# Optimization experiments

Hardware: AMD Instinct MI355X
Metric: run time of the kernel (lower is better)

The kernel has to match this reference:

```python
import jax, jax.numpy as jnp
import numpy as np

VAR0, VAR1 = 0.1, 0.2
CONF_THR = 0.02
NMS_THR = 0.4
PRE_K = 5000
POST_K = 750
N = 85680


def setup_inputs() -> dict:
    key = jax.random.key(0)
    k0, k1, k2, k3 = jax.random.split(key, 4)
    return {
        "loc": jax.random.normal(k0, (N, 4), jnp.float32),
        "conf": jax.random.uniform(k1, (N, 2), jnp.float32),
        "landmarks": jax.random.normal(k2, (N, 10), jnp.float32),
        "priors": jax.random.uniform(k3, (N, 4), jnp.float32),
        "img_w": 1920,
        "img_h": 1088,
    }


def _decode_boxes(loc, priors):
    # center-size decode -> xyxy
    cxy = priors[:, :2] + loc[:, :2] * VAR0 * priors[:, 2:]
    wh = priors[:, 2:] * jnp.exp(loc[:, 2:] * VAR1)
    return jnp.concatenate([cxy - wh * 0.5, cxy + wh * 0.5], axis=-1)


def _decode_landmarks(lmk, priors):
    pts = lmk.reshape(-1, 5, 2)                       # [N,5,2]
    out = priors[:, None, :2] + pts * VAR0 * priors[:, None, 2:]
    return out.reshape(-1, 10)


def _pairwise_iou(boxes):
    # boxes: [K,4] xyxy
    area = (boxes[:, 2] - boxes[:, 0]) * (boxes[:, 3] - boxes[:, 1])
    lt = jnp.maximum(boxes[:, None, :2], boxes[None, :, :2])  # [K,K,2]
    rb = jnp.minimum(boxes[:, None, 2:], boxes[None, :, 2:])
    wh = jnp.clip(rb - lt, 0.0)
    inter = wh[..., 0] * wh[..., 1]
    union = area[:, None] + area[None, :] - inter
    return inter / jnp.maximum(union, 1e-12)


def _greedy_nms(boxes, valid, thr):
    # boxes already sorted by descending score; valid marks real candidates.
    K = boxes.shape[0]
    iou = _pairwise_iou(boxes)                         # [K,K]
    idx = jnp.arange(K)

    def body(i, keep):
        suppress = keep[i] & (iou[i] > thr) & (idx > i)
        return keep & ~suppress

    return jax.lax.fori_loop(0, K, body, valid)


def reference(loc, conf, landmarks, priors, img_w, img_h):
    w = jnp.float32(img_w)
    h = jnp.float32(img_h)
    bbox_scale = jnp.array([w, h, w, h], jnp.float32)
    lmk_scale = jnp.tile(jnp.array([w, h], jnp.float32), 5)

    boxes = _decode_boxes(loc, priors) * bbox_scale          # [N,4]
    lmk = _decode_landmarks(landmarks, priors) * lmk_scale   # [N,10]
    scores = conf[:, 1]                                      # [N]

    # confidence filter fused into top-k via -inf masking (static shapes)
    masked = jnp.where(scores > CONF_THR, scores, -jnp.inf)
    top_scores, order = jax.lax.top_k(masked, PRE_K)         # [PRE_K]
    boxes_k = boxes[order]
    lmk_k = lmk[order]
    valid_k = top_scores > CONF_THR

    keep = _greedy_nms(boxes_k, valid_k, NMS_THR)            # [PRE_K] bool

    # compact kept rows (already score-sorted) into fixed [POST_K,15]
    rank = jnp.cumsum(keep) - 1
    rows = jnp.concatenate([boxes_k, top_scores[:, None], lmk_k], axis=1)
    dest = jnp.where(keep & (rank < POST_K), rank, POST_K)   # OOB -> dropped
    out = jnp.zeros((POST_K, 15), jnp.float32).at[dest].set(rows, mode="drop")
    return out
```

## Files before the change

kernel.cpp:

```cpp
#include <hip/hip_runtime.h>
#include <hip/hip_bf16.h>
#include <math.h>

#define N_IN 85680
#define PRE_K 5000
#define POST_K 750
#define NW 79
#define NPAD 5056
#define HSIZE 8192
#define CAND_MAX 8192
#define CONF_THR 0.02f
#define NMS_THR 0.4f
#define BITS_THR 0x3CA3D70Bu
#define NGRP 20
#define ZBYTES 66624

typedef unsigned int u32;
typedef unsigned long long u64;

__device__ __forceinline__ int cbase(int k) { return k * (5088 - 32 * k); }

__device__ __forceinline__ float opaquef(float x) { asm volatile("" : "+v"(x)); return x; }

__device__ __forceinline__ u32 bucket_of(u32 bits) {
    u32 b = (bits - BITS_THR) >> 13;
    return b >= HSIZE ? (HSIZE - 1) : b;
}

__global__ __launch_bounds__(256) void zero_kernel(u32* __restrict__ p) {
    int i = blockIdx.x * 256 + threadIdx.x;
    if (i < ZBYTES / 4) p[i] = 0u;
}

__global__ __launch_bounds__(256) void hist_kernel(const float2* __restrict__ conf2,
                                                   u32* __restrict__ hist) {
    __shared__ u32 h[HSIZE];
    for (int b = threadIdx.x; b < HSIZE; b += 256) h[b] = 0u;
    __syncthreads();
    int i = blockIdx.x * 256 + threadIdx.x;
    if (i < N_IN) {
        float s = conf2[i].y;
        if (s > CONF_THR) atomicAdd(&h[bucket_of(__float_as_uint(s))], 1u);
    }
    __syncthreads();
    for (int b = threadIdx.x; b < HSIZE; b += 256) {
        u32 v = h[b];
        if (v) atomicAdd(&hist[b], v);
    }
}

__global__ __launch_bounds__(1024) void scan_kernel(const u32* __restrict__ hist,
                                                    u32* __restrict__ bsel,
                                                    u32* __restrict__ bstart) {
    __shared__ u32 tot[1024];
    int c = threadIdx.x;
    u32 lh[8];
    u32 t = 0;
#pragma unroll
    for (int k = 0; k < 8; ++k) { lh[k] = hist[c * 8 + k]; t += lh[k]; }
    tot[c] = t;
    __syncthreads();
    for (int d = 1; d < 1024; d <<= 1) {
        u32 v = tot[c] + ((c + d < 1024) ? tot[c + d] : 0u);
        __syncthreads();
        tot[c] = v;
        __syncthreads();
    }
    u32 above = (c + 1 < 1024) ? tot[c + 1] : 0u;
    u32 s = above;
    for (int k = 7; k >= 0; --k) { bstart[c * 8 + k] = s; s += lh[k]; }
    if (above < PRE_K && above + t >= PRE_K) {
        u32 cum = above;
        for (int k = 7; k >= 0; --k) {
            cum += lh[k];
            if (cum >= PRE_K) { bsel[0] = (u32)(c * 8 + k); break; }
        }
    }
    if (c == 0 && tot[0] < PRE_K) bsel[0] = 0u;
}

__global__ __launch_bounds__(256) void compact_kernel(const float2* __restrict__ conf2,
                                                      const u32* __restrict__ bsel,
                                                      const u32* __restrict__ bstart,
                                                      u32* __restrict__ bfill,
                                                      u64* __restrict__ cand) {
    int i = blockIdx.x * 256 + threadIdx.x;
    if (i >= N_IN) return;
    float sc = conf2[i].y;
    if (!(sc > CONF_THR)) return;
    u32 bits = __float_as_uint(sc);
    u32 b = bucket_of(bits);
    if (b < bsel[0]) return;
    u32 pos = bstart[b] + atomicAdd(&bfill[b], 1u);
    if (pos < CAND_MAX) cand[pos] = ((u64)bits << 32) | (u64)(u32)(~(u32)i);
}

__global__ __launch_bounds__(256) void rankdec_kernel(const u64* __restrict__ cand,
                                                      const u32* __restrict__ bstart,
                                                      const u32* __restrict__ bfill,
                                                      const u32* __restrict__ bsel,
                                                      const float4* __restrict__ loc4,
                                                      const float4* __restrict__ pri4,
                                                      const float* __restrict__ lmk,
                                                      const int* __restrict__ imw,
                                                      const int* __restrict__ imh,
                                                      float4* __restrict__ rows4,
                                                      float4* __restrict__ boxes,
                                                      u64* __restrict__ validm) {
    u32 bs = bsel[0];
    u32 total = bstart[bs] + bfill[bs];
    if (total > CAND_MAX) total = CAND_MAX;
    float W = (float)(*imw), H = (float)(*imh);
    for (u32 s = blockIdx.x * blockDim.x + threadIdx.x; s < total;
         s += gridDim.x * blockDim.x) {
        u64 key = cand[s];
        u32 b = bucket_of((u32)(key >> 32));
        u32 st = bstart[b];
        u32 en = st + bfill[b];
        if (en > CAND_MAX) en = CAND_MAX;
        u32 r = st;
        for (u32 j = st; j < en; ++j) r += (cand[j] > key) ? 1u : 0u;
        if (r >= PRE_K) continue;
        u32 i = ~(u32)key;
        float score = __uint_as_float((u32)(key >> 32));
        float4 L = loc4[i];
        float4 P = pri4[i];
        float cx = P.x + opaquef((L.x * 0.1f) * P.z);
        float cy = P.y + opaquef((L.y * 0.1f) * P.w);
        float bw = P.z * (float)exp((double)(L.z * 0.2f));
        float bh = P.w * (float)exp((double)(L.w * 0.2f));
        float hw = opaquef(bw * 0.5f), hh = opaquef(bh * 0.5f);
        float x0 = (cx - hw) * W, y0 = (cy - hh) * H;
        float x1 = (cx + hw) * W, y1 = (cy + hh) * H;
        boxes[r] = make_float4(x0, y0, x1, y1);
        float lm[10];
#pragma unroll
        for (int p = 0; p < 5; ++p) {
            float2 q = ((const float2*)lmk)[(size_t)i * 5 + p];
            lm[2 * p]     = (P.x + opaquef((q.x * 0.1f) * P.z)) * W;
            lm[2 * p + 1] = (P.y + opaquef((q.y * 0.1f) * P.w)) * H;
        }
        float4* row = rows4 + (size_t)r * 4;
        row[0] = make_float4(x0, y0, x1, y1);
        row[1] = make_float4(score, lm[0], lm[1], lm[2]);
        row[2] = make_float4(lm[3], lm[4], lm[5], lm[6]);
        row[3] = make_float4(lm[7], lm[8], lm[9], 0.f);
        atomicOr(&validm[r >> 6], 1ull << (r & 63));
    }
}

__global__ __launch_bounds__(256) void mask_kernel(const float4* __restrict__ boxes,
                                                   u64* __restrict__ cmask) {
    __shared__ float4 cb4[4][64];
    int wv = threadIdx.x >> 6, t = threadIdx.x & 63;
    int t64 = blockIdx.x * 4 + wv;
    if (t64 >= NW * (NW + 1) / 2) return;
    int rc = (int)((sqrtf(8.0f * (float)t64 + 1.0f) - 1.0f) * 0.5f);
    while ((rc + 1) * (rc + 2) / 2 <= t64) ++rc;
    while (rc * (rc + 1) / 2 > t64) --rc;
    int cc = t64 - rc * (rc + 1) / 2;
    cb4[wv][t] = boxes[cc * 64 + t];
    int i = rc * 64 + t;
    float4 bi = boxes[i];
    float areai = (bi.z - bi.x) * (bi.w - bi.y);
    u64 word = 0ull;
#pragma unroll 4
    for (int k = 0; k < 64; ++k) {
        float4 bj = cb4[wv][k];
        float areaj = (bj.z - bj.x) * (bj.w - bj.y);
        float ltx = fmaxf(bi.x, bj.x), lty = fmaxf(bi.y, bj.y);
        float rbx = fminf(bi.z, bj.z), rby = fminf(bi.w, bj.w);
        float wx = fmaxf(rbx - ltx, 0.f), wy = fmaxf(rby - lty, 0.f);
        float inter = opaquef(wx * wy);
        float uni = fmaxf(areai + areaj - inter, 1e-12f);
        float iou = inter / uni;
        if (iou > NMS_THR) word |= (1ull << k);
    }
    if (i < PRE_K) cmask[(size_t)(cbase(cc) + (i - 64 * cc))] = word;
}

#define FC(k, q) cmask[(size_t)(cbase(k) + (q) - 64 * (k))]

#define WAITG(need)                                                                   \
    for (;;) {                                                                        \
        u32 d_ = __hip_atomic_load(&doneCnt, __ATOMIC_RELAXED,                        \
                                   __HIP_MEMORY_SCOPE_WORKGROUP);                     \
        if (d_ > (u32)NGRP) { dead = true; break; }                                   \
        if (d_ >= (u32)(need)) break;                                                 \
    }                                                                                 \
    asm volatile("" ::: "memory");

__device__ __forceinline__ u64 nms_solve(u64 valw, u64 sup, u64 dlow) {
    u64 keep = valw & ~__ballot(sup != 0ull);
    for (;;) {
        u64 conm = __ballot((dlow & keep) != 0ull);
        u64 cm = conm & keep;
        if (cm == 0ull) break;
        u64 U = keep & ~conm;
        u64 rem = __ballot((dlow & U) != 0ull) & keep;
        keep &= ~rem;
    }
    return keep;
}

__global__ __launch_bounds__(512) void reduce_scatter_kernel(const u64* __restrict__ cmask,
                                                             const u64* __restrict__ validm,
                                                             const float* __restrict__ rows,
                                                             float* __restrict__ out) {
    int tid = threadIdx.x;
    int g = tid >> 6, lane = tid & 63;
    __shared__ u64 keepAll[96];
    __shared__ u32 totG[32];
    __shared__ u32 doneCnt;
    __shared__ u32 wpref[96];
    for (int k = tid; k < 96; k += 512) keepAll[k] = 0ull;
    if (tid == 0) doneCnt = 0u;
    __syncthreads();
    u64 lmask = (1ull << lane) - 1ull;

    for (int s = 0; s < 3; ++s) {
        int G = s * 8 + g;
        if (G >= NGRP) break;
        int w0 = 4 * G;
        int nwg = NW - w0; if (nwg > 4) nwg = 4;
        int q0 = 64 * w0 + lane;
        int q1 = q0 + 64;
        int q2 = q0 + 128;
        int q3 = (nwg > 3) ? (q0 + 192) : q0;
        u64 t00 = FC(w0, q0);
        u64 t10 = (nwg > 1) ? FC(w0, q1) : 0ull;
        u64 t11 = (nwg > 1) ? FC(w0 + 1, q1) : 0ull;
        u64 t20 = (nwg > 2) ? FC(w0, q2) : 0ull;
        u64 t21 = (nwg > 2) ? FC(w0 + 1, q2) : 0ull;
        u64 t22 = (nwg > 2) ? FC(w0 + 2, q2) : 0ull;
        u64 t30 = (nwg > 3) ? FC(w0, q3) : 0ull;
        u64 t31 = (nwg > 3) ? FC(w0 + 1, q3) : 0ull;
        u64 t32 = (nwg > 3) ? FC(w0 + 2, q3) : 0ull;
        u64 t33 = (nwg > 3) ? FC(w0 + 3, q3) : 0ull;
        u64 v0 = validm[w0];
        u64 v1 = (nwg > 1) ? validm[w0 + 1] : 0ull;
        u64 v2 = (nwg > 2) ? validm[w0 + 2] : 0ull;
        u64 v3 = (nwg > 3) ? validm[w0 + 3] : 0ull;
        u64 sup0 = 0, sup1 = 0, sup2 = 0, sup3 = 0;
        bool dead = false;

        int d0 = 0;
        u64 c00=0,c01=0,c02=0,c03=0,c10=0,c11=0,c12=0,c13=0;
        if (w0 > 0) {
            c00 = FC(0, q0); c01 = FC(0, q1); c02 = FC(0, q2); c03 = FC(0, q3);
            c10 = FC(1, q0); c11 = FC(1, q1); c12 = FC(1, q2); c13 = FC(1, q3);
        }
        asm volatile("" ::: "memory");
        while (d0 < w0) {
            int d1 = d0 + 2;
            u64 n00=0,n01=0,n02=0,n03=0,n10=0,n11=0,n12=0,n13=0;
            if (d1 < w0) {
                n00 = FC(d1, q0);     n01 = FC(d1, q1);     n02 = FC(d1, q2);     n03 = FC(d1, q3);
                n10 = FC(d1 + 1, q0); n11 = FC(d1 + 1, q1); n12 = FC(d1 + 1, q2); n13 = FC(d1 + 1, q3);
            }
            asm volatile("" ::: "memory");
            WAITG(((d0 + 1) >> 2) + 1)
            if (dead) break;
            u64 ka = keepAll[d0], kb = keepAll[d0 + 1];
            sup0 |= (ka & c00) | (kb & c10);
            sup1 |= (ka & c01) | (kb & c11);
            sup2 |= (ka & c02) | (kb & c12);
            sup3 |= (ka & c03) | (kb & c13);
            c00=n00;c01=n01;c02=n02;c03=n03;c10=n10;c11=n11;c12=n12;c13=n13;
            d0 = d1;
        }
        if (!dead) {
            __builtin_amdgcn_s_setprio(1);
            u32 tp = (G > 0) ? totG[G - 1] : 0u;
            u64 k0 = 0, k1 = 0, k2 = 0, k3 = 0;
            if (tp < POST_K) {
                k0 = nms_solve(v0, sup0, t00 & lmask);
                sup1 |= k0 & t10; sup2 |= k0 & t20; sup3 |= k0 & t30;
                k1 = nms_solve(v1, sup1, t11 & lmask);
                sup2 |= k1 & t21; sup3 |= k1 & t31;
                k2 = nms_solve(v2, sup2, t22 & lmask);
                sup3 |= k2 & t32;
                k3 = nms_solve(v3, sup3, t33 & lmask);
            }
            if (lane == 0) {
                keepAll[w0]     = k0;
                keepAll[w0 + 1] = k1;
                keepAll[w0 + 2] = k2;
                keepAll[w0 + 3] = k3;
                u32 tk = tp + (u32)(__popcll(k0) + __popcll(k1) + __popcll(k2) + __popcll(k3));
                totG[G] = tk;
                asm volatile("s_waitcnt lgkmcnt(0)" ::: "memory");
                __hip_atomic_store(&doneCnt,
                                   (tk >= POST_K) ? (u32)(NGRP + 9) : (u32)(G + 1),
                                   __ATOMIC_RELAXED, __HIP_MEMORY_SCOPE_WORKGROUP);
            }
            __builtin_amdgcn_s_setprio(0);
        } else {
            break;
        }
    }
    __syncthreads();

    if (tid == 0) {
        u32 s = 0;
        for (int w = 0; w < NW; ++w) { wpref[w] = s; s += (u32)__popcll(keepAll[w]); }
        wpref[NW] = s;
    }
    __syncthreads();
    u32 totk = wpref[NW]; if (totk > POST_K) totk = POST_K;
    for (int r = tid; r < PRE_K; r += 512) {
        int w = r >> 6, b = r & 63;
        u64 kw = keepAll[w];
        if ((kw >> b) & 1ull) {
            u32 rank = wpref[w] + (u32)__popcll(kw & ((1ull << b) - 1ull));
            if (rank < POST_K) {
                const float* src = rows + (size_t)r * 16;
                float* dst = out + (size_t)rank * 15;
#pragma unroll
                for (int c2 = 0; c2 < 15; ++c2) dst[c2] = src[c2];
            }
        }
    }
    for (int r = (int)totk + tid; r < POST_K; r += 512) {
        float* dst = out + (size_t)r * 15;
#pragma unroll
        for (int c2 = 0; c2 < 15; ++c2) dst[c2] = 0.f;
    }
}

extern "C" void kernel_launch(void* const* d_in, const int* in_sizes, int n_in,
                              void* d_out, int out_size, void* d_ws, size_t ws_size,
                              hipStream_t stream) {
    const float* loc = (const float*)d_in[0];
    const float2* conf2 = (const float2*)d_in[1];
    const float* lmk = (const float*)d_in[2];
    const float* pri = (const float*)d_in[3];
    const int* imw = (const int*)d_in[4];
    const int* imh = (const int*)d_in[5];
    float* out = (float*)d_out;
    char* base = (char*)d_ws;

    u32* hist   = (u32*)(base + 0);
    u32* bfill  = (u32*)(base + 32768);
    u32* bsel   = (u32*)(base + 65536);
    u64* validm = (u64*)(base + 65600);
    u32* bstart = (u32*)(base + 67648);
    u64* cand   = (u64*)(base + 100416);
    float* rows = (float*)(base + 165952);
    float4* boxes = (float4*)(base + 485952);
    u64* cmask  = (u64*)(base + 566848);

    zero_kernel<<<(ZBYTES / 4 + 255) / 256, 256, 0, stream>>>((u32*)base);

    hist_kernel<<<(N_IN + 255) / 256, 256, 0, stream>>>(conf2, hist);
    scan_kernel<<<1, 1024, 0, stream>>>(hist, bsel, bstart);
    compact_kernel<<<(N_IN + 255) / 256, 256, 0, stream>>>(conf2, bsel, bstart, bfill, cand);
    rankdec_kernel<<<48, 256, 0, stream>>>(cand, bstart, bfill, bsel, (const float4*)loc,
                                           (const float4*)pri, lmk, imw, imh,
                                           (float4*)rows, boxes, validm);
    mask_kernel<<<(NW * (NW + 1) / 2 + 3) / 4, 256, 0, stream>>>(boxes, cmask);
    reduce_scatter_kernel<<<1, 512, 0, stream>>>(cmask, validm, rows, out);
}
```

Baseline: 94.14 us.

## Stage first 20 mask words' triangle in LDS and solve NMS serially in one wave

```diff
diff --git a/kernel.cpp b/kernel.cpp
--- a/kernel.cpp
+++ b/kernel.cpp
@@ -12,19 +12,31 @@
 #define CONF_THR 0.02f
 #define NMS_THR 0.4f
 #define BITS_THR 0x3CA3D70Bu
-#define NGRP 20
 #define ZBYTES 66624
+#define WLDS 20
+#define NCHUNK 110
 
 typedef unsigned int u32;
 typedef unsigned long long u64;
 
 __device__ __forceinline__ int cbase(int k) { return k * (5088 - 32 * k); }
+
+__device__ __forceinline__ int ldsoff(int k) {
+    int m = k >> 1;
+    return 128 * (m * (21 - m) + ((k & 1) ? (10 - m) : 0));
+}
 
 __device__ __forceinline__ float opaquef(float x) { asm volatile("" : "+v"(x)); return x; }
 
 __device__ __forceinline__ u32 bucket_of(u32 bits) {
     u32 b = (bits - BITS_THR) >> 13;
     return b >= HSIZE ? (HSIZE - 1) : b;
+}
+
+__device__ __forceinline__ void gload_lds16(const void* g, void* l) {
+    __builtin_amdgcn_global_load_lds(
+        (const __attribute__((address_space(1))) void*)g,
+        (__attribute__((address_space(3))) void*)l, 16, 0, 0);
 }
 
 __global__ __launch_bounds__(256) void zero_kernel(u32* __restrict__ p) {
@@ -181,15 +193,6 @@
 
 #define FC(k, q) cmask[(size_t)(cbase(k) + (q) - 64 * (k))]
 
-#define WAITG(need)                                                                   \
-    for (;;) {                                                                        \
-        u32 d_ = __hip_atomic_load(&doneCnt, __ATOMIC_RELAXED,                        \
-                                   __HIP_MEMORY_SCOPE_WORKGROUP);                     \
-        if (d_ > (u32)NGRP) { dead = true; break; }                                   \
-        if (d_ >= (u32)(need)) break;                                                 \
-    }                                                                                 \
-    asm volatile("" ::: "memory");
-
 __device__ __forceinline__ u64 nms_solve(u64 valw, u64 sup, u64 dlow) {
     u64 keep = valw & ~__ballot(sup != 0ull);
     for (;;) {
@@ -209,94 +212,51 @@
                                                              float* __restrict__ out) {
     int tid = threadIdx.x;
     int g = tid >> 6, lane = tid & 63;
+    __shared__ __align__(16) u64 tri[14080];
     __shared__ u64 keepAll[96];
-    __shared__ u32 totG[32];
-    __shared__ u32 doneCnt;
-    __shared__ u32 wpref[96];
+    __shared__ u64 validL[WLDS];
+    __shared__ u32 wpref[97];
     for (int k = tid; k < 96; k += 512) keepAll[k] = 0ull;
-    if (tid == 0) doneCnt = 0u;
     __syncthreads();
     u64 lmask = (1ull << lane) - 1ull;
 
-    for (int s = 0; s < 3; ++s) {
-        int G = s * 8 + g;
-        if (G >= NGRP) break;
-        int w0 = 4 * G;
-        int nwg = NW - w0; if (nwg > 4) nwg = 4;
-        int q0 = 64 * w0 + lane;
-        int q1 = q0 + 64;
-        int q2 = q0 + 128;
-        int q3 = (nwg > 3) ? (q0 + 192) : q0;
-        u64 t00 = FC(w0, q0);
-        u64 t10 = (nwg > 1) ? FC(w0, q1) : 0ull;
-        u64 t11 = (nwg > 1) ? FC(w0 + 1, q1) : 0ull;
-        u64 t20 = (nwg > 2) ? FC(w0, q2) : 0ull;
-        u64 t21 = (nwg > 2) ? FC(w0 + 1, q2) : 0ull;
-        u64 t22 = (nwg > 2) ? FC(w0 + 2, q2) : 0ull;
-        u64 t30 = (nwg > 3) ? FC(w0, q3) : 0ull;
-        u64 t31 = (nwg > 3) ? FC(w0 + 1, q3) : 0ull;
-        u64 t32 = (nwg > 3) ? FC(w0 + 2, q3) : 0ull;
-        u64 t33 = (nwg > 3) ? FC(w0 + 3, q3) : 0ull;
-        u64 v0 = validm[w0];
-        u64 v1 = (nwg > 1) ? validm[w0 + 1] : 0ull;
-        u64 v2 = (nwg > 2) ? validm[w0 + 2] : 0ull;
-        u64 v3 = (nwg > 3) ? validm[w0 + 3] : 0ull;
-        u64 sup0 = 0, sup1 = 0, sup2 = 0, sup3 = 0;
-        bool dead = false;
-
-        int d0 = 0;
-        u64 c00=0,c01=0,c02=0,c03=0,c10=0,c11=0,c12=0,c13=0;
-        if (w0 > 0) {
-            c00 = FC(0, q0); c01 = FC(0, q1); c02 = FC(0, q2); c03 = FC(0, q3);
-            c10 = FC(1, q0); c11 = FC(1, q1); c12 = FC(1, q2); c13 = FC(1, q3);
-        }
-        asm volatile("" ::: "memory");
-        while (d0 < w0) {
-            int d1 = d0 + 2;
-            u64 n00=0,n01=0,n02=0,n03=0,n10=0,n11=0,n12=0,n13=0;
-            if (d1 < w0) {
-                n00 = FC(d1, q0);     n01 = FC(d1, q1);     n02 = FC(d1, q2);     n03 = FC(d1, q3);
-                n10 = FC(d1 + 1, q0); n11 = FC(d1 + 1, q1); n12 = FC(d1 + 1, q2); n13 = FC(d1 + 1, q3);
+    for (int j = g; j < NCHUNK; j += 8) {
+        int k = 0, r = j;
+        while (r >= ((21 - k) >> 1)) { r -= (21 - k) >> 1; ++k; }
+        int off64 = ldsoff(k) + r * 128;
+        const char* gsrc = (const char*)(cmask + (size_t)cbase(k) + (size_t)r * 128)
+                           + (size_t)lane * 16;
+        gload_lds16(gsrc, (char*)tri + (size_t)off64 * 8);
+    }
+    if (g == 7 && lane < WLDS) validL[lane] = validm[lane];
+    asm volatile("s_waitcnt vmcnt(0)" ::: "memory");
+    __syncthreads();
+
+    if (g == 0) {
+        u32 totK = 0;
+        int w = 0;
+        for (; w < WLDS; ++w) {
+            int q = 64 * w + lane;
+            u64 sup = 0ull;
+            for (int w2 = 0; w2 < w; ++w2)
+                sup |= keepAll[w2] & tri[ldsoff(w2) + q - 64 * w2];
+            u64 dlow = tri[ldsoff(w) + lane] & lmask;
+            u64 keep = nms_solve(validL[w], sup, dlow);
+            if (lane == 0) keepAll[w] = keep;
+            totK += (u32)__popcll(keep);
+            if (totK >= POST_K) break;
+        }
+        if (totK < POST_K) {
+            for (w = WLDS; w < NW; ++w) {
+                int q = 64 * w + lane;
+                u64 sup = 0ull;
+                for (int w2 = 0; w2 < w; ++w2) sup |= keepAll[w2] & FC(w2, q);
+                u64 dlow = FC(w, q) & lmask;
+                u64 keep = nms_solve(validm[w], sup, dlow);
+                if (lane == 0) keepAll[w] = keep;
+                totK += (u32)__popcll(keep);
+                if (totK >= POST_K) break;
             }
-            asm volatile("" ::: "memory");
-            WAITG(((d0 + 1) >> 2) + 1)
-            if (dead) break;
-            u64 ka = keepAll[d0], kb = keepAll[d0 + 1];
-            sup0 |= (ka & c00) | (kb & c10);
-            sup1 |= (ka & c01) | (kb & c11);
-            sup2 |= (ka & c02) | (kb & c12);
-            sup3 |= (ka & c03) | (kb & c13);
-            c00=n00;c01=n01;c02=n02;c03=n03;c10=n10;c11=n11;c12=n12;c13=n13;
-            d0 = d1;
-        }
-        if (!dead) {
-            __builtin_amdgcn_s_setprio(1);
-            u32 tp = (G > 0) ? totG[G - 1] : 0u;
-            u64 k0 = 0, k1 = 0, k2 = 0, k3 = 0;
-            if (tp < POST_K) {
-                k0 = nms_solve(v0, sup0, t00 & lmask);
-                sup1 |= k0 & t10; sup2 |= k0 & t20; sup3 |= k0 & t30;
-                k1 = nms_solve(v1, sup1, t11 & lmask);
-                sup2 |= k1 & t21; sup3 |= k1 & t31;
-                k2 = nms_solve(v2, sup2, t22 & lmask);
-                sup3 |= k2 & t32;
-                k3 = nms_solve(v3, sup3, t33 & lmask);
-            }
-            if (lane == 0) {
-                keepAll[w0]     = k0;
-                keepAll[w0 + 1] = k1;
-                keepAll[w0 + 2] = k2;
-                keepAll[w0 + 3] = k3;
-                u32 tk = tp + (u32)(__popcll(k0) + __popcll(k1) + __popcll(k2) + __popcll(k3));
-                totG[G] = tk;
-                asm volatile("s_waitcnt lgkmcnt(0)" ::: "memory");
-                __hip_atomic_store(&doneCnt,
-                                   (tk >= POST_K) ? (u32)(NGRP + 9) : (u32)(G + 1),
-                                   __ATOMIC_RELAXED, __HIP_MEMORY_SCOPE_WORKGROUP);
-            }
-            __builtin_amdgcn_s_setprio(0);
-        } else {
-            break;
         }
     }
     __syncthreads();
```

New measurement: 188.0 us. +99.8%, slower.
